# Performance work log

Hardware: AMD Instinct MI355X
Metric: run time of the kernel (lower is better)

Reference implementation:

```python
import jax, jax.numpy as jnp
import numpy as np

BETA = 0.25


def setup_inputs() -> dict:
    key = jax.random.key(0)
    k1, k2 = jax.random.split(key)
    z = jax.random.normal(k1, (16, 2048, 64), dtype=jnp.float32)
    emb = jax.random.uniform(k2, (8192, 64), dtype=jnp.float32)  # uniform_() init
    return {"z": z, "emb": emb}


def reference(z, emb):
    # z: [B, N, D], emb: [K, D]; use_norm=False so norm is identity.
    B, N, D = z.shape
    zf = z.reshape(-1, D)                                   # [B*N, D]
    # Squared euclidean distances; argmin is identical to cdist(p=2) argmin.
    d2 = (
        jnp.sum(zf * zf, axis=1, keepdims=True)
        - 2.0 * (zf @ emb.T)
        + jnp.sum(emb * emb, axis=1)
    )                                                       # [B*N, K]
    idx = jnp.argmin(d2, axis=1)                            # [B*N]
    z_q = emb[idx].reshape(z.shape)                         # [B, N, D]
    loss = BETA * jnp.mean((jax.lax.stop_gradient(z_q) - z) ** 2) + jnp.mean(
        (z_q - jax.lax.stop_gradient(z)) ** 2
    )
    z_q_st = z + jax.lax.stop_gradient(z_q - z)             # straight-through
    return z_q_st, idx, loss
```

## Files before the change

### kernel.cpp

```cpp
#include <hip/hip_runtime.h>
#include <hip/hip_bf16.h>
#include <math.h>

#define D 64
#define K_CODES 8192
#define M_QUERIES 32768
#define SLICES 8
#define CODES_PER_SLICE (K_CODES / SLICES)
#define CHUNK 32
#define NCHUNK (CODES_PER_SLICE / CHUNK)
#define QPB 256
#define TAU_V 4e-3f

typedef __attribute__((ext_vector_type(8))) short bf16x8;
typedef __attribute__((ext_vector_type(4))) float f32x4;
typedef __attribute__((ext_vector_type(16))) float f32x16;

__device__ __forceinline__ unsigned short f2bf(float x) {
    __hip_bfloat16 h = __float2bfloat16(x);
    return *reinterpret_cast<unsigned short*>(&h);
}
__device__ __forceinline__ float bf2f(unsigned short s) {
    __hip_bfloat16 h;
    *reinterpret_cast<unsigned short*>(&h) = s;
    return __bfloat162float(h);
}
__device__ __forceinline__ void gld_lds16(const void* g, void* l) {
    __builtin_amdgcn_global_load_lds(
        (const __attribute__((address_space(1))) void*)g,
        (__attribute__((address_space(3))) void*)l, 16, 0, 0);
}
__device__ __forceinline__ void gld_lds4(const void* g, void* l) {
    __builtin_amdgcn_global_load_lds(
        (const __attribute__((address_space(1))) void*)g,
        (__attribute__((address_space(3))) void*)l, 4, 0, 0);
}

__global__ __launch_bounds__(256) void k0_split(const float* __restrict__ emb,
                                                unsigned short* __restrict__ e_hi,
                                                unsigned short* __restrict__ e_lo,
                                                float* __restrict__ halfee,
                                                int* __restrict__ ws_cnt) {
    const int t = threadIdx.x;
    const int grp = blockIdx.x;
    if (grp == 0 && t == 0) *ws_cnt = 0;
    const int u = t & 7;
#pragma unroll
    for (int it = 0; it < 2; ++it) {
        const int r = (t >> 3) + it * 32;
        const int code = grp * 64 + r;
        const float* src = emb + ((size_t)code * 64 + u * 8);
        float4 f0 = *(const float4*)(src);
        float4 f1 = *(const float4*)(src + 4);
        float f[8] = {f0.x, f0.y, f0.z, f0.w, f1.x, f1.y, f1.z, f1.w};
        bf16x8 h, lo;
        float s = 0.f;
#pragma unroll
        for (int j = 0; j < 8; ++j) {
            float e = f[j];
            s += e * e;
            unsigned short hh = f2bf(e);
            h[j]  = (short)hh;
            lo[j] = (short)f2bf(e - bf2f(hh));
        }
        const int c32 = code >> 5, r32 = code & 31;
        size_t off = (size_t)c32 * 4096 + (size_t)(u * 32 + r32) * 16;
        *(bf16x8*)((char*)e_hi + off) = h;
        *(bf16x8*)((char*)e_lo + off) = lo;
        s += __shfl_xor(s, 1);
        s += __shfl_xor(s, 2);
        s += __shfl_xor(s, 4);
        if (u == 0) halfee[code] = 0.5f * s + 128.0f;
    }
}

__global__ __launch_bounds__(256, 1) void k1_mfma(const float* __restrict__ z,
                                                  const unsigned short* __restrict__ e_hi,
                                                  const unsigned short* __restrict__ e_lo,
                                                  const float* __restrict__ halfee,
                                                  float4* __restrict__ ws_part) {
    __shared__ __align__(16) unsigned short ldshi[2][CHUNK * 64];
    __shared__ __align__(16) unsigned short ldslo[2][CHUNK * 64];
    __shared__ __align__(16) float ldshe[2][CHUNK];

    const int tid = threadIdx.x;
    const int wid = tid >> 6;
    const int l   = tid & 63;
    const int col = l & 31;
    const int hi  = l >> 5;
    const int slice = blockIdx.y;
    const int chunk0 = slice * NCHUNK;

    const int qw0 = blockIdx.x * QPB + wid * 64;
    bf16x8 qh[2][4], ql[2][4];
#pragma unroll
    for (int g = 0; g < 2; ++g) {
        const int qrow = qw0 + g * 32 + col;
#pragma unroll
        for (int kk = 0; kk < 4; ++kk) {
            const float* src = z + (size_t)qrow * D + kk * 16 + hi * 8;
            float4 f0 = *(const float4*)(src);
            float4 f1 = *(const float4*)(src + 4);
            float f[8] = {f0.x, f0.y, f0.z, f0.w, f1.x, f1.y, f1.z, f1.w};
            bf16x8 h, lo;
#pragma unroll
            for (int j = 0; j < 8; ++j) {
                float x = -f[j];
                unsigned short hh = f2bf(x);
                float r = x - bf2f(hh);
                h[j]  = (short)hh;
                lo[j] = (short)f2bf(r);
            }
            qh[g][kk] = h;
            ql[g][kk] = lo;
        }
    }

    float g1A = 1e30f, g2A = 1e30f; int giA = 0x7fffffff;
    float g1B = 1e30f, g2B = 1e30f; int giB = 0x7fffffff;

#define STAGE(buf, c1)                                                           \
    {                                                                            \
        size_t cb = (size_t)(chunk0 + (c1)) * 4096 + wid * 1024 + l * 16;        \
        gld_lds16((const char*)e_hi + cb, (char*)&ldshi[buf][0] + wid * 1024);   \
        gld_lds16((const char*)e_lo + cb, (char*)&ldslo[buf][0] + wid * 1024);   \
        if (tid < 32)                                                            \
            gld_lds4((const char*)halfee + (size_t)(chunk0 + (c1)) * 128 + tid * 4, \
                     (char*)&ldshe[buf][0]);                                     \
    }

#define TOP2(accX, g1X, g2X, giX, cbase)                                         \
    {                                                                            \
        float m1p = 1e30f, m2p = 1e30f;                                          \
        _Pragma("unroll") for (int r = 0; r < 16; ++r) {                         \
            float vp = __int_as_float((__float_as_int(accX[r]) & 0xFFFFFFF0) | r); \
            m2p = __builtin_amdgcn_fmed3f(vp, m1p, m2p);                         \
            m1p = fminf(m1p, vp);                                                \
        }                                                                        \
        int p1 = __float_as_int(m1p) & 15;                                       \
        int code = (cbase) + (p1 & 3) + 8 * (p1 >> 2) + 4 * hi;                  \
        bool lt = m1p < g1X;                                                     \
        g2X = fminf(lt ? g1X : g2X, lt ? m2p : m1p);                             \
        g1X = lt ? m1p : g1X;                                                    \
        giX = lt ? code : giX;                                                   \
    }

#define COMPUTE(bufc, cbase)                                                     \
    {                                                                            \
        const char*  bh  = (const char*)ldshi[bufc];                             \
        const char*  bl  = (const char*)ldslo[bufc];                             \
        const float* bhe = ldshe[bufc];                                          \
        f32x16 accA, accB;                                                       \
        _Pragma("unroll") for (int g4 = 0; g4 < 4; ++g4) {                       \
            f32x4 he4 = *(const f32x4*)(bhe + g4 * 8 + 4 * hi);                  \
            _Pragma("unroll") for (int j = 0; j < 4; ++j) {                      \
                accA[g4 * 4 + j] = he4[j];                                       \
                accB[g4 * 4 + j] = he4[j];                                       \
            }                                                                    \
        }                                                                        \
        _Pragma("unroll") for (int kk = 0; kk < 4; ++kk) {                       \
            int a0 = ((kk * 2 + hi) * 32 + col) * 16;       \
            bf16x8 ah = *(const bf16x8*)(bh + a0);                               \
            bf16x8 al = *(const bf16x8*)(bl + a0);                               \
            accA = __builtin_amdgcn_mfma_f32_32x32x16_bf16(ah, qh[0][kk], accA, 0, 0, 0); \
            accB = __builtin_amdgcn_mfma_f32_32x32x16_bf16(ah, qh[1][kk], accB, 0, 0, 0); \
            accA = __builtin_amdgcn_mfma_f32_32x32x16_bf16(ah, ql[0][kk], accA, 0, 0, 0); \
            accB = __builtin_amdgcn_mfma_f32_32x32x16_bf16(ah, ql[1][kk], accB, 0, 0, 0); \
            accA = __builtin_amdgcn_mfma_f32_32x32x16_bf16(al, qh[0][kk], accA, 0, 0, 0); \
            accB = __builtin_amdgcn_mfma_f32_32x32x16_bf16(al, qh[1][kk], accB, 0, 0, 0); \
        }                                                                        \
        TOP2(accA, g1A, g2A, giA, cbase);                                        \
        TOP2(accB, g1B, g2B, giB, cbase);                                        \
    }

    STAGE(0, 0);
    __syncthreads();
    for (int c = 0; c < NCHUNK; ++c) {
        const int cur = c & 1;
        if (c + 1 < NCHUNK) STAGE(cur ^ 1, c + 1);
        COMPUTE(cur, slice * CODES_PER_SLICE + c * CHUNK);
        __syncthreads();
    }

#pragma unroll
    for (int g = 0; g < 2; ++g) {
        float a1 = g ? g1B : g1A, a2 = g ? g2B : g2A;
        int   ai = g ? giB : giA;
        float o1 = __shfl_xor(a1, 32);
        float o2 = __shfl_xor(a2, 32);
        int   oi = __shfl_xor(ai, 32);
        bool  take = (o1 < a1) || (o1 == a1 && oi < ai);
        float n2   = take ? fminf(o2, a1) : fminf(a2, o1);
        a1 = take ? o1 : a1;
        ai = take ? oi : ai;
        a2 = n2;
        if (l < 32) {
            int q = qw0 + g * 32 + col;
            ws_part[(size_t)q * SLICES + slice] =
                make_float4(a1, a2, __int_as_float(ai), 0.f);
        }
    }
#undef STAGE
#undef TOP2
#undef COMPUTE
}

__global__ __launch_bounds__(256) void k1b_merge(const float4* __restrict__ ws_part,
                                                 int* __restrict__ ws_idx,
                                                 int* __restrict__ ws_cnt,
                                                 int* __restrict__ ws_list) {
    int q = blockIdx.x * blockDim.x + threadIdx.x;
    float m1 = 1e30f, m2 = 1e30f;
    int   i1 = 0x7fffffff;
#pragma unroll
    for (int s = 0; s < SLICES; ++s) {
        float4 p = ws_part[(size_t)q * SLICES + s];
        float v1 = p.x, v2 = p.y;
        int   vi = __float_as_int(p.z);
        if (v1 < m1 || (v1 == m1 && vi < i1)) { m2 = fminf(m1, v2); m1 = v1; i1 = vi; }
        else                                  { m2 = fminf(m2, v1); }
    }
    ws_idx[q] = i1;
    if (m2 - m1 < TAU_V) {
        int r = atomicAdd(ws_cnt, 1);
        ws_list[r] = q;
    }
}

__global__ __launch_bounds__(256) void k2_rescue(const float* __restrict__ z,
                                                 const float* __restrict__ emb,
                                                 const int* __restrict__ ws_cnt,
                                                 const int* __restrict__ ws_list,
                                                 int* __restrict__ ws_idx) {
    __shared__ float  zrow[D];
    __shared__ double rv[256];
    __shared__ int    ri[256];
    const int cnt = *ws_cnt;
    for (int r = blockIdx.x; r < cnt; r += gridDim.x) {
        const int q = ws_list[r];
        __syncthreads();
        if (threadIdx.x < D) zrow[threadIdx.x] = z[(size_t)q * D + threadIdx.x];
        __syncthreads();
        double best = 1e300;
        int    bi   = 0x7fffffff;
        for (int c = threadIdx.x; c < K_CODES; c += 256) {
            const float4* er = (const float4*)(emb + (size_t)c * D);
            double acc = 0.0;
#pragma unroll
            for (int k = 0; k < 16; ++k) {
                float4 e  = er[k];
                double d0 = (double)zrow[4 * k + 0] - (double)e.x;
                double d1 = (double)zrow[4 * k + 1] - (double)e.y;
                double d2 = (double)zrow[4 * k + 2] - (double)e.z;
                double d3 = (double)zrow[4 * k + 3] - (double)e.w;
                acc += d0 * d0 + d1 * d1 + d2 * d2 + d3 * d3;
            }
            if (acc < best) { best = acc; bi = c; }
        }
        rv[threadIdx.x] = best;
        ri[threadIdx.x] = bi;
        __syncthreads();
        for (int s = 128; s > 0; s >>= 1) {
            if (threadIdx.x < s) {
                double ov = rv[threadIdx.x + s];
                int    oi = ri[threadIdx.x + s];
                if (ov < rv[threadIdx.x] || (ov == rv[threadIdx.x] && oi < ri[threadIdx.x])) {
                    rv[threadIdx.x] = ov;
                    ri[threadIdx.x] = oi;
                }
            }
            __syncthreads();
        }
        if (threadIdx.x == 0) ws_idx[q] = ri[0];
        __syncthreads();
    }
}

__global__ __launch_bounds__(256) void k3_gather(const float* __restrict__ emb,
                                                 const float* __restrict__ z,
                                                 const int* __restrict__ ws_idx,
                                                 float* __restrict__ out,
                                                 float* __restrict__ partial) {
    __shared__ float sb[256];
    int g = blockIdx.x * 256 + threadIdx.x;
    int q = g >> 6, d = g & 63;
    int id = ws_idx[q];
    float e = emb[(size_t)id * D + d];
    out[g] = e;
    if (d == 0) out[(size_t)M_QUERIES * D + q] = (float)id;
    float df = e - z[g];
    sb[threadIdx.x] = df * df;
    __syncthreads();
    for (int s = 128; s > 0; s >>= 1) {
        if (threadIdx.x < s) sb[threadIdx.x] += sb[threadIdx.x + s];
        __syncthreads();
    }
    if (threadIdx.x == 0) partial[blockIdx.x] = sb[0];
}

__global__ __launch_bounds__(256) void k4_loss(const float* __restrict__ partial,
                                               float* __restrict__ out) {
    __shared__ double sb[256];
    double s = 0.0;
    for (int i = threadIdx.x; i < (M_QUERIES * D) / 256; i += 256) s += (double)partial[i];
    sb[threadIdx.x] = s;
    __syncthreads();
    for (int st = 128; st > 0; st >>= 1) {
        if (threadIdx.x < st) sb[threadIdx.x] += sb[threadIdx.x + st];
        __syncthreads();
    }
    if (threadIdx.x == 0)
        out[(size_t)M_QUERIES * D + M_QUERIES] =
            (float)(1.25 * sb[0] / (double)((size_t)M_QUERIES * D));
}

extern "C" void kernel_launch(void* const* d_in, const int* in_sizes, int n_in,
                              void* d_out, int out_size, void* d_ws, size_t ws_size,
                              hipStream_t stream) {
    const float* z   = (const float*)d_in[0];
    const float* emb = (const float*)d_in[1];
    float* out = (float*)d_out;
    char*  ws  = (char*)d_ws;

    unsigned short* e_hi    = (unsigned short*)(ws);
    unsigned short* e_lo    = (unsigned short*)(ws + 1048576);
    float*          halfee  = (float*)(ws + 2097152);
    float4*         ws_part = (float4*)(ws + 2129920);
    int*            ws_idx  = (int*)(ws + 2129920 + 4194304);
    int*            ws_cnt  = (int*)(ws + 2129920 + 4194304 + 131072);
    int*            ws_list = (int*)(ws + 2129920 + 4194304 + 131136);
    float*          partial = (float*)(ws + 2129920 + 4194304 + 262208);

    k0_split<<<K_CODES / 64, 256, 0, stream>>>(emb, e_hi, e_lo, halfee, ws_cnt);

    dim3 g1(M_QUERIES / QPB, SLICES);
    k1_mfma<<<g1, 256, 0, stream>>>(z, e_hi, e_lo, halfee, ws_part);

    k1b_merge<<<M_QUERIES / 256, 256, 0, stream>>>(ws_part, ws_idx, ws_cnt, ws_list);

    k2_rescue<<<256, 256, 0, stream>>>(z, emb, ws_cnt, ws_list, ws_idx);

    k3_gather<<<(M_QUERIES * D) / 256, 256, 0, stream>>>(emb, z, ws_idx, out, partial);

    k4_loss<<<1, 256, 0, stream>>>(partial, out);
}
```

Baseline: 193.9 us.

## Halve queries per wave and software-pipeline MFMA with tree top-2 reduction

```diff
diff --git a/kernel.cpp b/kernel.cpp
--- a/kernel.cpp
+++ b/kernel.cpp
@@ -9,7 +9,7 @@
 #define CODES_PER_SLICE (K_CODES / SLICES)
 #define CHUNK 32
 #define NCHUNK (CODES_PER_SLICE / CHUNK)
-#define QPB 256
+#define QPB 128
 #define TAU_V 4e-3f
 
 typedef __attribute__((ext_vector_type(8))) short bf16x8;
@@ -90,34 +90,32 @@
     const int hi  = l >> 5;
     const int slice = blockIdx.y;
     const int chunk0 = slice * NCHUNK;
-
-    const int qw0 = blockIdx.x * QPB + wid * 64;
-    bf16x8 qh[2][4], ql[2][4];
-#pragma unroll
-    for (int g = 0; g < 2; ++g) {
-        const int qrow = qw0 + g * 32 + col;
-#pragma unroll
-        for (int kk = 0; kk < 4; ++kk) {
-            const float* src = z + (size_t)qrow * D + kk * 16 + hi * 8;
-            float4 f0 = *(const float4*)(src);
-            float4 f1 = *(const float4*)(src + 4);
-            float f[8] = {f0.x, f0.y, f0.z, f0.w, f1.x, f1.y, f1.z, f1.w};
-            bf16x8 h, lo;
-#pragma unroll
-            for (int j = 0; j < 8; ++j) {
-                float x = -f[j];
-                unsigned short hh = f2bf(x);
-                float r = x - bf2f(hh);
-                h[j]  = (short)hh;
-                lo[j] = (short)f2bf(r);
-            }
-            qh[g][kk] = h;
-            ql[g][kk] = lo;
-        }
-    }
-
-    float g1A = 1e30f, g2A = 1e30f; int giA = 0x7fffffff;
-    float g1B = 1e30f, g2B = 1e30f; int giB = 0x7fffffff;
+    const int cbase0 = slice * CODES_PER_SLICE;
+
+    const int qw0 = blockIdx.x * QPB + wid * 32;
+    const int qrow = qw0 + col;
+    bf16x8 qh[4], ql[4];
+#pragma unroll
+    for (int kk = 0; kk < 4; ++kk) {
+        const float* src = z + (size_t)qrow * D + kk * 16 + hi * 8;
+        float4 f0 = *(const float4*)(src);
+        float4 f1 = *(const float4*)(src + 4);
+        float f[8] = {f0.x, f0.y, f0.z, f0.w, f1.x, f1.y, f1.z, f1.w};
+        bf16x8 h, lo;
+#pragma unroll
+        for (int j = 0; j < 8; ++j) {
+            float x = -f[j];
+            unsigned short hh = f2bf(x);
+            float r = x - bf2f(hh);
+            h[j]  = (short)hh;
+            lo[j] = (short)f2bf(r);
+        }
+        qh[kk] = h;
+        ql[kk] = lo;
+    }
+
+    float g1 = 1e30f, g2 = 1e30f;
+    int   gi = 0x7fffffff;
 
 #define STAGE(buf, c1)                                                           \
     {                                                                            \
@@ -129,80 +127,90 @@
                      (char*)&ldshe[buf][0]);                                     \
     }
 
-#define TOP2(accX, g1X, g2X, giX, cbase)                                         \
-    {                                                                            \
-        float m1p = 1e30f, m2p = 1e30f;                                          \
-        _Pragma("unroll") for (int r = 0; r < 16; ++r) {                         \
-            float vp = __int_as_float((__float_as_int(accX[r]) & 0xFFFFFFF0) | r); \
-            m2p = __builtin_amdgcn_fmed3f(vp, m1p, m2p);                         \
-            m1p = fminf(m1p, vp);                                                \
-        }                                                                        \
-        int p1 = __float_as_int(m1p) & 15;                                       \
-        int code = (cbase) + (p1 & 3) + 8 * (p1 >> 2) + 4 * hi;                  \
-        bool lt = m1p < g1X;                                                     \
-        g2X = fminf(lt ? g1X : g2X, lt ? m2p : m1p);                             \
-        g1X = lt ? m1p : g1X;                                                    \
-        giX = lt ? code : giX;                                                   \
-    }
-
-#define COMPUTE(bufc, cbase)                                                     \
+#define MFMA_CHUNK(bufc, acc)                                                    \
     {                                                                            \
         const char*  bh  = (const char*)ldshi[bufc];                             \
         const char*  bl  = (const char*)ldslo[bufc];                             \
         const float* bhe = ldshe[bufc];                                          \
-        f32x16 accA, accB;                                                       \
         _Pragma("unroll") for (int g4 = 0; g4 < 4; ++g4) {                       \
             f32x4 he4 = *(const f32x4*)(bhe + g4 * 8 + 4 * hi);                  \
-            _Pragma("unroll") for (int j = 0; j < 4; ++j) {                      \
-                accA[g4 * 4 + j] = he4[j];                                       \
-                accB[g4 * 4 + j] = he4[j];                                       \
-            }                                                                    \
+            _Pragma("unroll") for (int j = 0; j < 4; ++j)                        \
+                acc[g4 * 4 + j] = he4[j];                                        \
         }                                                                        \
         _Pragma("unroll") for (int kk = 0; kk < 4; ++kk) {                       \
             int a0 = ((kk * 2 + hi) * 32 + col) * 16;       \
             bf16x8 ah = *(const bf16x8*)(bh + a0);                               \
             bf16x8 al = *(const bf16x8*)(bl + a0);                               \
-            accA = __builtin_amdgcn_mfma_f32_32x32x16_bf16(ah, qh[0][kk], accA, 0, 0, 0); \
-            accB = __builtin_amdgcn_mfma_f32_32x32x16_bf16(ah, qh[1][kk], accB, 0, 0, 0); \
-            accA = __builtin_amdgcn_mfma_f32_32x32x16_bf16(ah, ql[0][kk], accA, 0, 0, 0); \
-            accB = __builtin_amdgcn_mfma_f32_32x32x16_bf16(ah, ql[1][kk], accB, 0, 0, 0); \
-            accA = __builtin_amdgcn_mfma_f32_32x32x16_bf16(al, qh[0][kk], accA, 0, 0, 0); \
-            accB = __builtin_amdgcn_mfma_f32_32x32x16_bf16(al, qh[1][kk], accB, 0, 0, 0); \
+            acc = __builtin_amdgcn_mfma_f32_32x32x16_bf16(ah, qh[kk], acc, 0, 0, 0); \
+            acc = __builtin_amdgcn_mfma_f32_32x32x16_bf16(ah, ql[kk], acc, 0, 0, 0); \
+            acc = __builtin_amdgcn_mfma_f32_32x32x16_bf16(al, qh[kk], acc, 0, 0, 0); \
         }                                                                        \
-        TOP2(accA, g1A, g2A, giA, cbase);                                        \
-        TOP2(accB, g1B, g2B, giB, cbase);                                        \
-    }
+    }
+
+#define TOP2T(acc, cbase)                                                        \
+    {                                                                            \
+        float t1[8], t2[8];                                                      \
+        _Pragma("unroll") for (int i = 0; i < 8; ++i) {                          \
+            float va = __int_as_float((__float_as_int(acc[2 * i])     & 0xFFFFFFF0) | (2 * i));     \
+            float vb = __int_as_float((__float_as_int(acc[2 * i + 1]) & 0xFFFFFFF0) | (2 * i + 1)); \
+            t1[i] = fminf(va, vb);                                               \
+            t2[i] = fmaxf(va, vb);                                               \
+        }                                                                        \
+        _Pragma("unroll") for (int s = 4; s > 0; s >>= 1) {                      \
+            _Pragma("unroll") for (int i = 0; i < s; ++i) {                      \
+                float m2c = fminf(t2[i], t2[i + s]);                             \
+                t2[i] = __builtin_amdgcn_fmed3f(t1[i], t1[i + s], m2c);          \
+                t1[i] = fminf(t1[i], t1[i + s]);                                 \
+            }                                                                    \
+        }                                                                        \
+        float m1p = t1[0], m2p = t2[0];                                          \
+        int p1 = __float_as_int(m1p) & 15;                                       \
+        int code = (cbase) + (p1 & 3) + 8 * (p1 >> 2) + 4 * hi;                  \
+        bool lt = m1p < g1;                                                      \
+        g2 = fminf(lt ? g1 : g2, lt ? m2p : m1p);                                \
+        g1 = lt ? m1p : g1;                                                      \
+        gi = lt ? code : gi;                                                     \
+    }
+
+    f32x16 accE, accO;
 
     STAGE(0, 0);
     __syncthreads();
-    for (int c = 0; c < NCHUNK; ++c) {
-        const int cur = c & 1;
-        if (c + 1 < NCHUNK) STAGE(cur ^ 1, c + 1);
-        COMPUTE(cur, slice * CODES_PER_SLICE + c * CHUNK);
-        __syncthreads();
-    }
-
-#pragma unroll
-    for (int g = 0; g < 2; ++g) {
-        float a1 = g ? g1B : g1A, a2 = g ? g2B : g2A;
-        int   ai = g ? giB : giA;
-        float o1 = __shfl_xor(a1, 32);
-        float o2 = __shfl_xor(a2, 32);
-        int   oi = __shfl_xor(ai, 32);
-        bool  take = (o1 < a1) || (o1 == a1 && oi < ai);
-        float n2   = take ? fminf(o2, a1) : fminf(a2, o1);
-        a1 = take ? o1 : a1;
-        ai = take ? oi : ai;
-        a2 = n2;
+    STAGE(1, 1);
+    MFMA_CHUNK(0, accE);
+    __syncthreads();
+    for (int cc = 1; cc + 1 < NCHUNK; cc += 2) {
+        STAGE(0, cc + 1);
+        MFMA_CHUNK(1, accO);
+        TOP2T(accE, cbase0 + (cc - 1) * CHUNK);
+        __syncthreads();
+        if (cc + 2 < NCHUNK) STAGE(1, cc + 2);
+        MFMA_CHUNK(0, accE);
+        TOP2T(accO, cbase0 + cc * CHUNK);
+        __syncthreads();
+    }
+    MFMA_CHUNK(1, accO);
+    TOP2T(accE, cbase0 + (NCHUNK - 2) * CHUNK);
+    TOP2T(accO, cbase0 + (NCHUNK - 1) * CHUNK);
+
+    {
+        float o1 = __shfl_xor(g1, 32);
+        float o2 = __shfl_xor(g2, 32);
+        int   oi = __shfl_xor(gi, 32);
+        bool  take = (o1 < g1) || (o1 == g1 && oi < gi);
+        float n2   = take ? fminf(o2, g1) : fminf(g2, o1);
+        g1 = take ? o1 : g1;
+        gi = take ? oi : gi;
+        g2 = n2;
         if (l < 32) {
-            int q = qw0 + g * 32 + col;
+            int q = qw0 + col;
             ws_part[(size_t)q * SLICES + slice] =
-                make_float4(a1, a2, __int_as_float(ai), 0.f);
+                make_float4(g1, g2, __int_as_float(gi), 0.f);
         }
     }
 #undef STAGE
-#undef TOP2
-#undef COMPUTE
+#undef MFMA_CHUNK
+#undef TOP2T
 }
 
 __global__ __launch_bounds__(256) void k1b_merge(const float4* __restrict__ ws_part,
```

New measurement: 195.8 us. About the same (+1.0%).
